# Optimization experiments

Hardware: AMD Instinct MI355X
Metric: run time of the kernel (lower is better)

## Reference

```python
import jax, jax.numpy as jnp
import numpy as np

ROLLBACK = 1  # rollback_range: warp at 2**rollback finer resolution, then downsample
B, C, H, W = 2, 32, 512, 512
CIN = 3 * (C // 2) + 2  # inner module input channels


def _bilinear_warp(img, res):
    """Bilinear gather. img: [B,Cc,Hh,Ww]; res: [B,Hh,Ww,2] pixel offsets (x,y).
    Samples img at (x+res_x, y+res_y) with zero padding outside."""
    Bb, Cc, Hh, Ww = img.shape
    gy, gx = jnp.meshgrid(jnp.arange(Hh, dtype=img.dtype),
                          jnp.arange(Ww, dtype=img.dtype), indexing='ij')
    sx = gx[None] + res[..., 0]  # [B,Hh,Ww]
    sy = gy[None] + res[..., 1]
    x0 = jnp.floor(sx); y0 = jnp.floor(sy)
    wx = sx - x0; wy = sy - y0

    def gather(yi, xi):
        inb = ((yi >= 0) & (yi < Hh) & (xi >= 0) & (xi < Ww)).astype(img.dtype)
        yc = jnp.clip(yi, 0, Hh - 1).astype(jnp.int32)
        xc = jnp.clip(xi, 0, Ww - 1).astype(jnp.int32)
        v = jax.vmap(lambda im, y, x: im[:, y, x])(img, yc, xc)  # [B,Cc,Hh,Ww]
        return v * inb[:, None]

    v00 = gather(y0, x0);     v01 = gather(y0, x0 + 1)
    v10 = gather(y0 + 1, x0); v11 = gather(y0 + 1, x0 + 1)
    wx = wx[:, None]; wy = wy[:, None]  # broadcast over channels
    return (v00 * (1 - wy) * (1 - wx) + v01 * (1 - wy) * wx
            + v10 * wy * (1 - wx) + v11 * wy * wx)


def _resize_img(img, f):  # [B,Cc,Hh,Ww] bilinear spatial resize
    Bb, Cc, Hh, Ww = img.shape
    return jax.image.resize(img, (Bb, Cc, int(Hh * f), int(Ww * f)), 'bilinear')


def _resize_res(res, f):  # [B,Hh,Ww,2]; pixel-unit values scale with resolution
    Bb, Hh, Ww, _ = res.shape
    return jax.image.resize(res, (Bb, int(Hh * f), int(Ww * f), 2), 'bilinear') * f


def res_warp_img(img, res, rollback):
    if rollback > 0:
        f = 2 ** rollback
        out = _bilinear_warp(_resize_img(img, f), _resize_res(res, f))
        return _resize_img(out, 1.0 / f)
    return _bilinear_warp(img, res)


def res_warp_res(res_a, res_b, rollback):
    # warp residual field a (treated as a 2-channel image, values in pixel units) by b
    if rollback > 0:
        f = 2 ** rollback
        a = _resize_res(res_a, f); b = _resize_res(res_b, f)
        out = jnp.transpose(_bilinear_warp(jnp.transpose(a, (0, 3, 1, 2)), b), (0, 2, 3, 1))
        return _resize_res(out, 1.0 / f)
    out = _bilinear_warp(jnp.transpose(res_a, (0, 3, 1, 2)), res_b)
    return jnp.transpose(out, (0, 2, 3, 1))


def combine_residuals(res_a, res_b, rollback):
    # flow composition: apply a then b
    return res_b + res_warp_res(res_a, res_b, rollback)


def _conv3x3(x, w, b):
    y = jax.lax.conv_general_dilated(x, w, (1, 1), 'SAME',
                                     dimension_numbers=('NCHW', 'OIHW', 'NCHW'))
    return y + b[None, :, None, None]


def setup_inputs() -> dict:
    key = jax.random.key(0)
    k1, k2, k3 = jax.random.split(key, 3)
    x = jax.random.normal(k1, (B, C, H, W), dtype=jnp.float32)
    res = jax.random.normal(k2, (B, 2, H, W), dtype=jnp.float32)  # ~1px flow
    W_inner = jax.random.normal(k3, (2, CIN, 3, 3), dtype=jnp.float32) * 0.02
    b_inner = jnp.zeros((2,), dtype=jnp.float32)
    return {"x": x, "res": res, "W_inner": W_inner, "b_inner": b_inner, "level": 0}


def reference(x, res, W_inner, b_inner, level):
    res_hw = jnp.transpose(res, (0, 2, 3, 1))  # [B,H,W,2]
    nf = x.shape[1]
    src, tgt = x[:, :nf // 2], x[:, nf // 2:]
    warped_tgt = res_warp_img(tgt, res_hw, ROLLBACK)
    bundle = jnp.concatenate([src, tgt, warped_tgt, res], axis=1)  # [B,3C/2+2,H,W]
    adj = _conv3x3(bundle, W_inner, b_inner)  # hindsight_adjustment [B,2,H,W]
    # mode == 'combine_res': state['down'][level]['input'] = combined residual
    new_res = combine_residuals(res_hw, jnp.transpose(adj, (0, 2, 3, 1)), ROLLBACK)
    hindsight_warped_tgt = res_warp_img(tgt, new_res, ROLLBACK)
    return jnp.concatenate([src, hindsight_warped_tgt], axis=1)  # [B,C,H,W]
```

## Files before the change

### kernel.cpp

```cpp
#include <hip/hip_runtime.h>
#include <hip/hip_bf16.h>
#include <cstdint>
#include <cstddef>

#define HW   512
#define HW2  1024
#define SZ   (512 * 512)
#define NPT  (34 * 34)
#define K_PTS 5

struct UpTap { int i0, i1; float w0, w1; };

__device__ __forceinline__ UpTap up_tap(int i) {
  UpTap t;
  int k = i >> 1;
  if ((i & 1) == 0) {
    t.i0 = k - 1; t.i1 = k; t.w0 = 0.25f; t.w1 = 0.75f;
    if (k == 0) { t.i0 = 0; t.w0 = 0.0f; t.w1 = 1.0f; }
  } else {
    t.i0 = k; t.i1 = k + 1; t.w0 = 0.75f; t.w1 = 0.25f;
    if (k == HW - 1) { t.i1 = HW - 1; t.w0 = 1.0f; t.w1 = 0.0f; }
  }
  return t;
}

__device__ __forceinline__ float up_at(const float* __restrict__ plane, int yi, int xi) {
  UpTap ty = up_tap(yi), tx = up_tap(xi);
  const float* r0 = plane + (size_t)ty.i0 * HW;
  const float* r1 = plane + (size_t)ty.i1 * HW;
  float v00 = r0[tx.i0], v01 = r0[tx.i1];
  float v10 = r1[tx.i0], v11 = r1[tx.i1];
  return ty.w0 * (tx.w0 * v00 + tx.w1 * v01) + ty.w1 * (tx.w0 * v10 + tx.w1 * v11);
}

__device__ __forceinline__ void axis_taps(float s, int& base, float& w0, float& w1, float& w2) {
  float f0 = floorf(s);
  int i0 = (int)f0;
  float fr = s - f0;
  int b = (i0 & 1) ? (i0 >> 1) : (i0 >> 1) - 1;
  b = b < 0 ? 0 : (b > (HW - 3) ? (HW - 3) : b);
  float w[3] = {0.0f, 0.0f, 0.0f};
  if ((unsigned)i0 < (unsigned)HW2) {
    UpTap t = up_tap(i0);
    w[t.i0 - b] += (1.0f - fr) * t.w0;
    w[t.i1 - b] += (1.0f - fr) * t.w1;
  }
  if ((unsigned)(i0 + 1) < (unsigned)HW2) {
    UpTap t = up_tap(i0 + 1);
    w[t.i0 - b] += fr * t.w0;
    w[t.i1 - b] += fr * t.w1;
  }
  base = b; w0 = w[0]; w1 = w[1]; w2 = w[2];
}

__global__ void copy_src_kernel(const float* __restrict__ x, float* __restrict__ out) {
  const size_t half = (size_t)16 * SZ;
  const size_t nvec = half / 4;
  size_t i = (size_t)blockIdx.x * blockDim.x + threadIdx.x;
  if (i < 2 * nvec) {
    size_t b = i / nvec, j = i % nvec;
    const float4* s = (const float4*)(x + b * 2 * half);
    float4* d = (float4*)(out + b * 2 * half);
    d[j] = s[j];
  }
}

struct PtTaps {
  int   off;
  float wy0, wy1, wy2, wx0, wx1, wx2;
};

__device__ __forceinline__ void compute_taps(const float* __restrict__ fx,
                                             const float* __restrict__ fy,
                                             float scale,
                                             int gx0, int gy0, int tid,
                                             PtTaps (&pt)[K_PTS]) {
  #pragma unroll
  for (int i = 0; i < K_PTS; ++i) {
    int p = tid + i * 256;
    pt[i].off = 0;
    pt[i].wy0 = pt[i].wy1 = pt[i].wy2 = 0.0f;
    pt[i].wx0 = pt[i].wx1 = pt[i].wx2 = 0.0f;
    if (p < NPT) {
      int ry = p / 34, rx = p % 34;
      int yy = gy0 + ry, xx = gx0 + rx;
      if ((unsigned)yy < (unsigned)HW2 && (unsigned)xx < (unsigned)HW2) {
        float sx = (float)xx + scale * up_at(fx, yy, xx);
        float sy = (float)yy + scale * up_at(fy, yy, xx);
        int bx, by;
        axis_taps(sx, bx, pt[i].wx0, pt[i].wx1, pt[i].wx2);
        axis_taps(sy, by, pt[i].wy0, pt[i].wy1, pt[i].wy2);
        pt[i].off = by * HW + bx;
      }
    }
  }
}

__device__ __forceinline__ float eval_taps(const float* __restrict__ plane, const PtTaps& t) {
  const float* p0 = plane + t.off;
  float r0 = t.wx0 * p0[0]        + t.wx1 * p0[1]        + t.wx2 * p0[2];
  float r1 = t.wx0 * p0[HW]       + t.wx1 * p0[HW + 1]   + t.wx2 * p0[HW + 2];
  float r2 = t.wx0 * p0[2 * HW]   + t.wx1 * p0[2 * HW + 1] + t.wx2 * p0[2 * HW + 2];
  return t.wy0 * r0 + t.wy1 * r1 + t.wy2 * r2;
}

__global__ void warp_img_kernel(const float* __restrict__ x,
                                const float* __restrict__ res,
                                float* __restrict__ out)
{
  __shared__ float s_tile[NPT];

  const int b = blockIdx.z;
  const int tx0 = blockIdx.x * 16, ty0 = blockIdx.y * 16;
  const int gx0 = tx0 * 2 - 1, gy0 = ty0 * 2 - 1;
  const int tid = threadIdx.x;

  const float* resx = res + (size_t)b * 2 * SZ;
  const float* resy = resx + SZ;

  PtTaps pt[K_PTS];
  compute_taps(resx, resy, 2.0f, gx0, gy0, tid, pt);

  const int ly = tid >> 4, lx = tid & 15;
  const int oy = ty0 + ly, ox = tx0 + lx;
  const float RW[4] = {0.25f, 0.75f, 0.75f, 0.25f};
  float wy[4], wx[4];
  float sumy = 0.f, sumx = 0.f;
  #pragma unroll
  for (int d = 0; d < 4; ++d) {
    int g = 2 * oy - 1 + d;
    wy[d] = ((unsigned)g < (unsigned)HW2) ? RW[d] : 0.0f; sumy += wy[d];
    g = 2 * ox - 1 + d;
    wx[d] = ((unsigned)g < (unsigned)HW2) ? RW[d] : 0.0f; sumx += wx[d];
  }
  const float inv = 1.0f / (sumy * sumx);

  for (int c = 0; c < 16; ++c) {
    const float* plane = x + ((size_t)b * 32 + 16 + c) * SZ;
    #pragma unroll
    for (int i = 0; i < K_PTS; ++i) {
      int p = tid + i * 256;
      if (p < NPT) s_tile[p] = eval_taps(plane, pt[i]);
    }
    __syncthreads();
    float acc = 0.0f;
    #pragma unroll
    for (int dy = 0; dy < 4; ++dy) {
      float rowacc = 0.0f;
      const float* row = &s_tile[(2 * ly + dy) * 34 + 2 * lx];
      #pragma unroll
      for (int dx = 0; dx < 4; ++dx) rowacc += wx[dx] * row[dx];
      acc += wy[dy] * rowacc;
    }
    acc *= inv;
    out[(((size_t)b * 32 + 16 + c) * HW + oy) * HW + ox] = acc;
    __syncthreads();
  }
}

__global__ void conv_kernel(const float* __restrict__ x,
                            const float* __restrict__ warped,
                            const float* __restrict__ res,
                            const float* __restrict__ Wc,
                            const float* __restrict__ bc,
                            float* __restrict__ adj)
{
  __shared__ float sw[900];
  const int tid = threadIdx.y * 16 + threadIdx.x;
  for (int i = tid; i < 900; i += 256) sw[i] = Wc[i];
  __syncthreads();

  const int b = blockIdx.z;
  const int oy = blockIdx.y * 16 + threadIdx.y;
  const int ox = blockIdx.x * 16 + threadIdx.x;

  float acc0 = bc[0];
  float acc1 = bc[1];

  for (int ic = 0; ic < 50; ++ic) {
    const float* w0 = &sw[ic * 9];
    const float* w1 = &sw[450 + ic * 9];
    const float* plane;
    if (ic < 32)      plane = x      + ((size_t)b * 32 + ic) * SZ;
    else if (ic < 48) plane = warped + ((size_t)b * 32 + 16 + (ic - 32)) * SZ;
    else              plane = res    + ((size_t)b * 2 + (ic - 48)) * SZ;
    #pragma unroll
    for (int ky = 0; ky < 3; ++ky) {
      int yy = oy + ky - 1;
      bool yok = (unsigned)yy < (unsigned)HW;
      #pragma unroll
      for (int kx = 0; kx < 3; ++kx) {
        int xx = ox + kx - 1;
        float v = 0.0f;
        if (yok && (unsigned)xx < (unsigned)HW)
          v = plane[(size_t)yy * HW + xx];
        acc0 += v * w0[ky * 3 + kx];
        acc1 += v * w1[ky * 3 + kx];
      }
    }
  }
  adj[((size_t)b * 2 + 0) * SZ + (size_t)oy * HW + ox] = acc0;
  adj[((size_t)b * 2 + 1) * SZ + (size_t)oy * HW + ox] = acc1;
}

__global__ void new_res_kernel(const float* __restrict__ res,
                               const float* __restrict__ adj,
                               float* __restrict__ nres)
{
  __shared__ float s_tile[NPT];

  const int b = blockIdx.z;
  const int tx0 = blockIdx.x * 16, ty0 = blockIdx.y * 16;
  const int gx0 = tx0 * 2 - 1, gy0 = ty0 * 2 - 1;
  const int tid = threadIdx.x;

  const float* adjx = adj + (size_t)b * 2 * SZ;
  const float* adjy = adjx + SZ;

  PtTaps pt[K_PTS];
  compute_taps(adjx, adjy, 2.0f, gx0, gy0, tid, pt);

  const int ly = tid >> 4, lx = tid & 15;
  const int oy = ty0 + ly, ox = tx0 + lx;
  const float RW[4] = {0.25f, 0.75f, 0.75f, 0.25f};
  float wy[4], wx[4];
  float sumy = 0.f, sumx = 0.f;
  #pragma unroll
  for (int d = 0; d < 4; ++d) {
    int g = 2 * oy - 1 + d;
    wy[d] = ((unsigned)g < (unsigned)HW2) ? RW[d] : 0.0f; sumy += wy[d];
    g = 2 * ox - 1 + d;
    wx[d] = ((unsigned)g < (unsigned)HW2) ? RW[d] : 0.0f; sumx += wx[d];
  }
  const float inv = 1.0f / (sumy * sumx);

  for (int c = 0; c < 2; ++c) {
    const float* plane = res + ((size_t)b * 2 + c) * SZ;
    #pragma unroll
    for (int i = 0; i < K_PTS; ++i) {
      int p = tid + i * 256;
      if (p < NPT) s_tile[p] = eval_taps(plane, pt[i]);
    }
    __syncthreads();
    float acc = 0.0f;
    #pragma unroll
    for (int dy = 0; dy < 4; ++dy) {
      float rowacc = 0.0f;
      const float* row = &s_tile[(2 * ly + dy) * 34 + 2 * lx];
      #pragma unroll
      for (int dx = 0; dx < 4; ++dx) rowacc += wx[dx] * row[dx];
      acc += wy[dy] * rowacc;
    }
    acc = acc * inv + adjx[((size_t)c) * SZ + (size_t)oy * HW + ox];
    nres[((size_t)b * 2 + c) * SZ + (size_t)oy * HW + ox] = acc;
    __syncthreads();
  }
}

extern "C" void kernel_launch(void* const* d_in, const int* in_sizes, int n_in,
                              void* d_out, int out_size, void* d_ws, size_t ws_size,
                              hipStream_t stream) {
  const float* x   = (const float*)d_in[0];
  const float* res = (const float*)d_in[1];
  const float* Wc  = (const float*)d_in[2];
  const float* bc  = (const float*)d_in[3];
  float* out = (float*)d_out;

  float* adj  = (float*)d_ws;
  float* nres = adj + (size_t)2 * 2 * SZ;

  {
    const size_t nvec = 2 * ((size_t)16 * SZ / 4);
    copy_src_kernel<<<dim3((unsigned)((nvec + 255) / 256)), dim3(256), 0, stream>>>(x, out);
  }

  dim3 tile_grid(32, 32, 2);

  warp_img_kernel<<<tile_grid, dim3(256), 0, stream>>>(x, res, out);

  conv_kernel<<<tile_grid, dim3(16, 16), 0, stream>>>(x, out, res, Wc, bc, adj);

  new_res_kernel<<<tile_grid, dim3(256), 0, stream>>>(res, adj, nres);

  warp_img_kernel<<<tile_grid, dim3(256), 0, stream>>>(x, nres, out);
}
```

Measured before the change: 447.1 us.

## Stage warp gather windows and conv input tiles in shared memory

```diff
diff --git a/kernel.cpp b/kernel.cpp
--- a/kernel.cpp
+++ b/kernel.cpp
@@ -8,6 +8,9 @@
 #define SZ   (512 * 512)
 #define NPT  (34 * 34)
 #define K_PTS 5
+#define WIN   44
+#define WS    45
+#define MARG  13
 
 struct UpTap { int i0, i1; float w0, w1; };
 
@@ -66,41 +69,52 @@
 }
 
 struct PtTaps {
-  int   off;
+  int   pk;
   float wy0, wy1, wy2, wx0, wx1, wx2;
 };
 
 __device__ __forceinline__ void compute_taps(const float* __restrict__ fx,
                                              const float* __restrict__ fy,
-                                             float scale,
-                                             int gx0, int gy0, int tid,
-                                             PtTaps (&pt)[K_PTS]) {
+                                             int gx0, int gy0, int cx0, int ry0,
+                                             int tid, PtTaps (&pt)[K_PTS]) {
   #pragma unroll
   for (int i = 0; i < K_PTS; ++i) {
     int p = tid + i * 256;
-    pt[i].off = 0;
+    pt[i].pk = 0;
     pt[i].wy0 = pt[i].wy1 = pt[i].wy2 = 0.0f;
     pt[i].wx0 = pt[i].wx1 = pt[i].wx2 = 0.0f;
     if (p < NPT) {
       int ry = p / 34, rx = p % 34;
       int yy = gy0 + ry, xx = gx0 + rx;
       if ((unsigned)yy < (unsigned)HW2 && (unsigned)xx < (unsigned)HW2) {
-        float sx = (float)xx + scale * up_at(fx, yy, xx);
-        float sy = (float)yy + scale * up_at(fy, yy, xx);
+        float sx = (float)xx + 2.0f * up_at(fx, yy, xx);
+        float sy = (float)yy + 2.0f * up_at(fy, yy, xx);
         int bx, by;
         axis_taps(sx, bx, pt[i].wx0, pt[i].wx1, pt[i].wx2);
         axis_taps(sy, by, pt[i].wy0, pt[i].wy1, pt[i].wy2);
-        pt[i].off = by * HW + bx;
+        pt[i].pk = ((by - ry0) << 16) | ((bx - cx0) & 0xffff);
       }
     }
   }
 }
 
-__device__ __forceinline__ float eval_taps(const float* __restrict__ plane, const PtTaps& t) {
-  const float* p0 = plane + t.off;
-  float r0 = t.wx0 * p0[0]        + t.wx1 * p0[1]        + t.wx2 * p0[2];
-  float r1 = t.wx0 * p0[HW]       + t.wx1 * p0[HW + 1]   + t.wx2 * p0[HW + 2];
-  float r2 = t.wx0 * p0[2 * HW]   + t.wx1 * p0[2 * HW + 1] + t.wx2 * p0[2 * HW + 2];
+__device__ __forceinline__ float eval_pt(const float* __restrict__ s_win,
+                                         const float* __restrict__ plane,
+                                         int cx0, int ry0, const PtTaps& t) {
+  int iy = t.pk >> 16;
+  int ix = (int)(short)(t.pk & 0xffff);
+  float r0, r1, r2;
+  if ((unsigned)iy <= (unsigned)(WIN - 3) && (unsigned)ix <= (unsigned)(WIN - 3)) {
+    const float* p = s_win + iy * WS + ix;
+    r0 = t.wx0 * p[0]      + t.wx1 * p[1]          + t.wx2 * p[2];
+    r1 = t.wx0 * p[WS]     + t.wx1 * p[WS + 1]     + t.wx2 * p[WS + 2];
+    r2 = t.wx0 * p[2 * WS] + t.wx1 * p[2 * WS + 1] + t.wx2 * p[2 * WS + 2];
+  } else {
+    const float* p = plane + (size_t)(ry0 + iy) * HW + (cx0 + ix);
+    r0 = t.wx0 * p[0]      + t.wx1 * p[1]          + t.wx2 * p[2];
+    r1 = t.wx0 * p[HW]     + t.wx1 * p[HW + 1]     + t.wx2 * p[HW + 2];
+    r2 = t.wx0 * p[2 * HW] + t.wx1 * p[2 * HW + 1] + t.wx2 * p[2 * HW + 2];
+  }
   return t.wy0 * r0 + t.wy1 * r1 + t.wy2 * r2;
 }
 
@@ -108,6 +122,7 @@
                                 const float* __restrict__ res,
                                 float* __restrict__ out)
 {
+  __shared__ float s_win[WIN * WS];
   __shared__ float s_tile[NPT];
 
   const int b = blockIdx.z;
@@ -115,11 +130,14 @@
   const int gx0 = tx0 * 2 - 1, gy0 = ty0 * 2 - 1;
   const int tid = threadIdx.x;
 
+  int cx0 = tx0 - MARG; cx0 = cx0 < 0 ? 0 : (cx0 > HW - WIN ? HW - WIN : cx0);
+  int ry0 = ty0 - MARG; ry0 = ry0 < 0 ? 0 : (ry0 > HW - WIN ? HW - WIN : ry0);
+
   const float* resx = res + (size_t)b * 2 * SZ;
   const float* resy = resx + SZ;
 
   PtTaps pt[K_PTS];
-  compute_taps(resx, resy, 2.0f, gx0, gy0, tid, pt);
+  compute_taps(resx, resy, gx0, gy0, cx0, ry0, tid, pt);
 
   const int ly = tid >> 4, lx = tid & 15;
   const int oy = ty0 + ly, ox = tx0 + lx;
@@ -137,10 +155,15 @@
 
   for (int c = 0; c < 16; ++c) {
     const float* plane = x + ((size_t)b * 32 + 16 + c) * SZ;
+    for (int i = tid; i < WIN * WIN; i += 256) {
+      int r = i / WIN, cc = i % WIN;
+      s_win[r * WS + cc] = plane[(size_t)(ry0 + r) * HW + (cx0 + cc)];
+    }
+    __syncthreads();
     #pragma unroll
     for (int i = 0; i < K_PTS; ++i) {
       int p = tid + i * 256;
-      if (p < NPT) s_tile[p] = eval_taps(plane, pt[i]);
+      if (p < NPT) s_tile[p] = eval_pt(s_win, plane, cx0, ry0, pt[i]);
     }
     __syncthreads();
     float acc = 0.0f;
@@ -154,10 +177,10 @@
     }
     acc *= inv;
     out[(((size_t)b * 32 + 16 + c) * HW + oy) * HW + ox] = acc;
-    __syncthreads();
-  }
-}
-
+  }
+}
+
+#define CTS 37
 __global__ void conv_kernel(const float* __restrict__ x,
                             const float* __restrict__ warped,
                             const float* __restrict__ res,
@@ -166,47 +189,67 @@
                             float* __restrict__ adj)
 {
   __shared__ float sw[900];
-  const int tid = threadIdx.y * 16 + threadIdx.x;
+  __shared__ float s_ch[34 * CTS];
+  const int tid = threadIdx.x;
   for (int i = tid; i < 900; i += 256) sw[i] = Wc[i];
-  __syncthreads();
 
   const int b = blockIdx.z;
-  const int oy = blockIdx.y * 16 + threadIdx.y;
-  const int ox = blockIdx.x * 16 + threadIdx.x;
-
-  float acc0 = bc[0];
-  float acc1 = bc[1];
+  const int oy0 = blockIdx.y * 32, ox0 = blockIdx.x * 32;
+  const int lr = tid >> 3;
+  const int lc = (tid & 7) * 4;
+
+  float a0[4] = {0, 0, 0, 0}, a1[4] = {0, 0, 0, 0};
 
   for (int ic = 0; ic < 50; ++ic) {
-    const float* w0 = &sw[ic * 9];
-    const float* w1 = &sw[450 + ic * 9];
     const float* plane;
     if (ic < 32)      plane = x      + ((size_t)b * 32 + ic) * SZ;
     else if (ic < 48) plane = warped + ((size_t)b * 32 + 16 + (ic - 32)) * SZ;
     else              plane = res    + ((size_t)b * 2 + (ic - 48)) * SZ;
+    __syncthreads();
+    for (int i = tid; i < 34 * 34; i += 256) {
+      int r = i / 34, c = i % 34;
+      int gy = oy0 - 1 + r, gx = ox0 - 1 + c;
+      float v = 0.0f;
+      if ((unsigned)gy < (unsigned)HW && (unsigned)gx < (unsigned)HW)
+        v = plane[(size_t)gy * HW + gx];
+      s_ch[r * CTS + c] = v;
+    }
+    __syncthreads();
+    const float* w0 = &sw[ic * 9];
+    const float* w1 = &sw[450 + ic * 9];
+    float win[3][6];
     #pragma unroll
     for (int ky = 0; ky < 3; ++ky) {
-      int yy = oy + ky - 1;
-      bool yok = (unsigned)yy < (unsigned)HW;
+      const float* rowp = &s_ch[(lr + ky) * CTS + lc];
       #pragma unroll
-      for (int kx = 0; kx < 3; ++kx) {
-        int xx = ox + kx - 1;
-        float v = 0.0f;
-        if (yok && (unsigned)xx < (unsigned)HW)
-          v = plane[(size_t)yy * HW + xx];
-        acc0 += v * w0[ky * 3 + kx];
-        acc1 += v * w1[ky * 3 + kx];
+      for (int j = 0; j < 6; ++j) win[ky][j] = rowp[j];
+    }
+    #pragma unroll
+    for (int j = 0; j < 4; ++j) {
+      #pragma unroll
+      for (int ky = 0; ky < 3; ++ky) {
+        #pragma unroll
+        for (int kx = 0; kx < 3; ++kx) {
+          float v = win[ky][j + kx];
+          a0[j] += v * w0[ky * 3 + kx];
+          a1[j] += v * w1[ky * 3 + kx];
+        }
       }
     }
   }
-  adj[((size_t)b * 2 + 0) * SZ + (size_t)oy * HW + ox] = acc0;
-  adj[((size_t)b * 2 + 1) * SZ + (size_t)oy * HW + ox] = acc1;
+  const float b0 = bc[0], b1 = bc[1];
+  const int oy = oy0 + lr, ox = ox0 + lc;
+  float4 o0 = make_float4(a0[0] + b0, a0[1] + b0, a0[2] + b0, a0[3] + b0);
+  float4 o1 = make_float4(a1[0] + b1, a1[1] + b1, a1[2] + b1, a1[3] + b1);
+  *(float4*)&adj[((size_t)b * 2 + 0) * SZ + (size_t)oy * HW + ox] = o0;
+  *(float4*)&adj[((size_t)b * 2 + 1) * SZ + (size_t)oy * HW + ox] = o1;
 }
 
 __global__ void new_res_kernel(const float* __restrict__ res,
                                const float* __restrict__ adj,
                                float* __restrict__ nres)
 {
+  __shared__ float s_win[WIN * WS];
   __shared__ float s_tile[NPT];
 
   const int b = blockIdx.z;
@@ -214,11 +257,14 @@
   const int gx0 = tx0 * 2 - 1, gy0 = ty0 * 2 - 1;
   const int tid = threadIdx.x;
 
+  int cx0 = tx0 - MARG; cx0 = cx0 < 0 ? 0 : (cx0 > HW - WIN ? HW - WIN : cx0);
+  int ry0 = ty0 - MARG; ry0 = ry0 < 0 ? 0 : (ry0 > HW - WIN ? HW - WIN : ry0);
+
   const float* adjx = adj + (size_t)b * 2 * SZ;
   const float* adjy = adjx + SZ;
 
   PtTaps pt[K_PTS];
-  compute_taps(adjx, adjy, 2.0f, gx0, gy0, tid, pt);
+  compute_taps(adjx, adjy, gx0, gy0, cx0, ry0, tid, pt);
 
   const int ly = tid >> 4, lx = tid & 15;
   const int oy = ty0 + ly, ox = tx0 + lx;
@@ -236,10 +282,15 @@
 
   for (int c = 0; c < 2; ++c) {
     const float* plane = res + ((size_t)b * 2 + c) * SZ;
+    for (int i = tid; i < WIN * WIN; i += 256) {
+      int r = i / WIN, cc = i % WIN;
+      s_win[r * WS + cc] = plane[(size_t)(ry0 + r) * HW + (cx0 + cc)];
+    }
+    __syncthreads();
     #pragma unroll
     for (int i = 0; i < K_PTS; ++i) {
       int p = tid + i * 256;
-      if (p < NPT) s_tile[p] = eval_taps(plane, pt[i]);
+      if (p < NPT) s_tile[p] = eval_pt(s_win, plane, cx0, ry0, pt[i]);
     }
     __syncthreads();
     float acc = 0.0f;
@@ -278,7 +329,7 @@
 
   warp_img_kernel<<<tile_grid, dim3(256), 0, stream>>>(x, res, out);
 
-  conv_kernel<<<tile_grid, dim3(16, 16), 0, stream>>>(x, out, res, Wc, bc, adj);
+  conv_kernel<<<dim3(16, 16, 2), dim3(256), 0, stream>>>(x, out, res, Wc, bc, adj);
 
   new_res_kernel<<<tile_grid, dim3(256), 0, stream>>>(res, adj, nres);
 
```

Result: slower. 530.5 us (+18.7%).
